# Kernel tuning notes

Hardware: AMD Instinct MI355X
Metric: run time of the kernel (lower is better)

## Reference

```python
import jax, jax.numpy as jnp
import numpy as np
from jax import lax

GAP_PENALTY = 0.0
TEMPERATURE = 1.0
B, A, L, D, K = 64, 26, 384, 512, 18


def setup_inputs() -> dict:
    key = jax.random.key(0)
    k1, k2, k3, k4 = jax.random.split(key, 4)
    matrices = jax.random.normal(k1, (B, A, L), dtype=jnp.float32)
    # ragged lengths: (len_i, len_0) per pair, in [L//2, L]
    shapes = jax.random.randint(k2, (B, 2), L // 2, L + 1, dtype=jnp.int32)
    s = 1.0 / np.sqrt(A * K)  # torch Conv1d default init scale
    conv_w = jax.random.uniform(k3, (D, A, K), minval=-s, maxval=s, dtype=jnp.float32)
    conv_b = jax.random.uniform(k4, (D,), minval=-s, maxval=s, dtype=jnp.float32)
    return {"matrices": matrices, "shapes": shapes, "conv_w": conv_w, "conv_b": conv_b}


def _smoothmax3(a, b, c, t):
    # t * log(exp(a/t) + exp(b/t) + exp(c/t)), numerically stable
    m = jnp.maximum(jnp.maximum(a, b), c)
    return m + t * jnp.log(jnp.exp((a - m) / t) + jnp.exp((b - m) / t) + jnp.exp((c - m) / t))


def _nw_matrix(sim, t, g):
    # sim: (L, L). Returns smoothed NW value matrix V: (L+1, L+1).
    # V[i,j] = sim[i-1,j-1] + smoothmax(V[i-1,j-1], V[i-1,j]-g, V[i,j-1]-g)
    n = sim.shape[0]
    row0 = -g * jnp.arange(n + 1, dtype=sim.dtype)  # free/affine leading gaps on top row

    def row_step(prev_row, inp):
        s_row, i = inp  # s_row: (L,)
        v_left0 = -g * i  # V[i, 0]

        def col_step(left, xs):
            s, diag, up = xs
            v = s + _smoothmax3(diag, up - g, left - g, t)
            return v, v

        _, rest = lax.scan(col_step, v_left0, (s_row, prev_row[:-1], prev_row[1:]))
        new_row = jnp.concatenate([v_left0[None], rest])
        return new_row, new_row

    _, rows = lax.scan(row_step, row0, (sim, jnp.arange(1, n + 1, dtype=sim.dtype)))
    return jnp.concatenate([row0[None], rows], axis=0)


def needleman_wunsch(sim, shapes, gap_penalty, temperature):
    # sim: (B, L, L) similarity vs sequence 0; shapes: (B, 2) int lengths.
    # Soft alignment posterior = grad of smoothed terminal score wrt similarity.
    li = jnp.clip(shapes[:, 0], 0, sim.shape[1])
    lj = jnp.clip(shapes[:, 1], 0, sim.shape[2])

    def total_score(s):
        V = jax.vmap(lambda m: _nw_matrix(m, temperature, gap_penalty))(s)  # (B, L+1, L+1)
        b = jnp.arange(s.shape[0])
        return jnp.sum(V[b, li, lj])

    return jax.grad(total_score)(sim)  # (B, L, L), expected match matrix


def reference(matrices, shapes, conv_w, conv_b):
    # Conv1d padding='same' with even kernel: torch pads (k-1)//2 left, k//2 right
    k = conv_w.shape[-1]
    pad = ((k - 1) // 2, k // 2)
    emb = lax.conv_general_dilated(
        matrices, conv_w, window_strides=(1,), padding=[pad],
        dimension_numbers=("NCH", "OIH", "NCH"),
    ) + conv_b[None, :, None]  # (B, D, L)
    e = jnp.transpose(emb, (0, 2, 1))  # (B, L, D)
    sim = jnp.einsum("bld,md->blm", e, e[0])  # (B, L_i, L_0): similarity vs sequence 0
    align = needleman_wunsch(sim, shapes, GAP_PENALTY, TEMPERATURE)  # (B, L, L)
    m = jnp.transpose(matrices, (0, 2, 1))  # (B, L, A)
    # consensus in sequence-0 coordinates, then project back to each sequence
    consensus = jnp.mean(jnp.einsum("nia,nij->nja", m, align), axis=0)  # (L, A)
    return jnp.einsum("ja,nij->nia", consensus, align)  # (B, L, A)
```

## Files before the change

kernel.cpp:

```cpp
#include <hip/hip_runtime.h>
#include <hip/hip_bf16.h>
#include <math.h>

#define B_  64
#define A_  26
#define L_  384
#define D_  512
#define K_  18
#define LP1 385
#define VS  384

typedef __attribute__((ext_vector_type(8))) short bf16x8;
typedef __attribute__((ext_vector_type(4))) float f32x4;
typedef unsigned short ushort_t;
typedef unsigned int uint_t;

__device__ __forceinline__ ushort_t f2bf(float v) {
    uint_t u = __float_as_uint(v);
    uint_t r = (u + 0x7FFFu + ((u >> 16) & 1u)) >> 16;
    return (ushort_t)r;
}

__device__ __forceinline__ float dpp_up1(float x) {
    return __int_as_float(__builtin_amdgcn_update_dpp(
        0, __float_as_int(x), 0x138, 0xF, 0xF, true));
}
__device__ __forceinline__ float dpp_down1(float x) {
    return __int_as_float(__builtin_amdgcn_update_dpp(
        0, __float_as_int(x), 0x130, 0xF, 0xF, true));
}

__global__ void transpose_w_kernel(const float* __restrict__ w, float* __restrict__ wt) {
    int o = blockIdx.x * blockDim.x + threadIdx.x;
    int total = A_ * K_ * D_;
    if (o >= total) return;
    int d = o % D_;
    int r = o / D_;
    wt[o] = w[(size_t)d * (A_ * K_) + r];
}

__global__ __launch_bounds__(512) void conv_kernel(const float* __restrict__ x,
                                                   const float* __restrict__ wt,
                                                   const float* __restrict__ bias,
                                                   ushort_t* __restrict__ ehi,
                                                   ushort_t* __restrict__ elo) {
    const int TL = 32;
    const int XW = TL + K_ - 1;
    int l0 = blockIdx.x * TL;
    int b  = blockIdx.y;
    int d  = threadIdx.x;
    __shared__ float xs[A_][XW];
    for (int idx = threadIdx.x; idx < A_ * XW; idx += 512) {
        int a = idx / XW, p = idx % XW;
        int g = l0 - (K_ - 1) / 2 + p;
        xs[a][p] = (g >= 0 && g < L_) ? x[((size_t)b * A_ + a) * L_ + g] : 0.0f;
    }
    __syncthreads();
    float acc[TL];
#pragma unroll
    for (int l = 0; l < TL; ++l) acc[l] = 0.0f;
#pragma unroll 1
    for (int a = 0; a < A_; ++a) {
        float xr[XW];
#pragma unroll
        for (int p = 0; p < XW; ++p) xr[p] = xs[a][p];
        const float* wrow = wt + (size_t)(a * K_) * D_ + d;
#pragma unroll
        for (int k = 0; k < K_; ++k) {
            float w = wrow[(size_t)k * D_];
#pragma unroll
            for (int l = 0; l < TL; ++l)
                acc[l] = fmaf(xr[k + l], w, acc[l]);
        }
    }
    float bv = bias[d];
#pragma unroll
    for (int l = 0; l < TL; ++l) {
        float v = acc[l] + bv;
        ushort_t h = f2bf(v);
        float hf = __uint_as_float(((uint_t)h) << 16);
        ushort_t lo = f2bf(v - hf);
        size_t idx = ((size_t)b * L_ + (l0 + l)) * D_ + d;
        ehi[idx] = h;
        elo[idx] = lo;
    }
}

__global__ __launch_bounds__(256) void sim_kernel(const ushort_t* __restrict__ ehi,
                                                  const ushort_t* __restrict__ elo,
                                                  float* __restrict__ sim) {
    int b = blockIdx.z;
    int w = threadIdx.x >> 6;
    int lane = threadIdx.x & 63;
    int l0 = blockIdx.y * 64 + 32 * (w >> 1);
    int m0 = blockIdx.x * 64 + 32 * (w & 1);
    int r = lane & 15, g = lane >> 4;
    size_t rowA = ((size_t)b * L_ + l0 + r) * D_ + g * 8;
    size_t rowB = ((size_t)m0 + r) * D_ + g * 8;
    const ushort_t* pah = ehi + rowA;
    const ushort_t* pal = elo + rowA;
    const ushort_t* pbh = ehi + rowB;
    const ushort_t* pbl = elo + rowB;
    f32x4 acc00 = {0.f, 0.f, 0.f, 0.f}, acc01 = acc00, acc10 = acc00, acc11 = acc00;
#pragma unroll 2
    for (int ks = 0; ks < 16; ++ks) {
        int off = ks * 32;
        bf16x8 Ah0 = *(const bf16x8*)(pah + off);
        bf16x8 Ah1 = *(const bf16x8*)(pah + 16 * D_ + off);
        bf16x8 Al0 = *(const bf16x8*)(pal + off);
        bf16x8 Al1 = *(const bf16x8*)(pal + 16 * D_ + off);
        bf16x8 Bh0 = *(const bf16x8*)(pbh + off);
        bf16x8 Bh1 = *(const bf16x8*)(pbh + 16 * D_ + off);
        bf16x8 Bl0 = *(const bf16x8*)(pbl + off);
        bf16x8 Bl1 = *(const bf16x8*)(pbl + 16 * D_ + off);
        acc00 = __builtin_amdgcn_mfma_f32_16x16x32_bf16(Ah0, Bh0, acc00, 0, 0, 0);
        acc00 = __builtin_amdgcn_mfma_f32_16x16x32_bf16(Ah0, Bl0, acc00, 0, 0, 0);
        acc00 = __builtin_amdgcn_mfma_f32_16x16x32_bf16(Al0, Bh0, acc00, 0, 0, 0);
        acc01 = __builtin_amdgcn_mfma_f32_16x16x32_bf16(Ah0, Bh1, acc01, 0, 0, 0);
        acc01 = __builtin_amdgcn_mfma_f32_16x16x32_bf16(Ah0, Bl1, acc01, 0, 0, 0);
        acc01 = __builtin_amdgcn_mfma_f32_16x16x32_bf16(Al0, Bh1, acc01, 0, 0, 0);
        acc10 = __builtin_amdgcn_mfma_f32_16x16x32_bf16(Ah1, Bh0, acc10, 0, 0, 0);
        acc10 = __builtin_amdgcn_mfma_f32_16x16x32_bf16(Ah1, Bl0, acc10, 0, 0, 0);
        acc10 = __builtin_amdgcn_mfma_f32_16x16x32_bf16(Al1, Bh0, acc10, 0, 0, 0);
        acc11 = __builtin_amdgcn_mfma_f32_16x16x32_bf16(Ah1, Bh1, acc11, 0, 0, 0);
        acc11 = __builtin_amdgcn_mfma_f32_16x16x32_bf16(Ah1, Bl1, acc11, 0, 0, 0);
        acc11 = __builtin_amdgcn_mfma_f32_16x16x32_bf16(Al1, Bh1, acc11, 0, 0, 0);
    }
    float* sp = sim + ((size_t)b * L_ + l0) * L_ + m0;
#pragma unroll
    for (int v = 0; v < 4; ++v) {
        int row = g * 4 + v;
        sp[(size_t)row * L_ + r]             = acc00[v];
        sp[(size_t)row * L_ + 16 + r]        = acc01[v];
        sp[(size_t)(16 + row) * L_ + r]      = acc10[v];
        sp[(size_t)(16 + row) * L_ + 16 + r] = acc11[v];
    }
}

__global__ __launch_bounds__(64, 1) void nw_fwd_kernel(const float* __restrict__ sim, float* __restrict__ V) {
    int b = blockIdx.x;
    int l = threadIdx.x;
    const float* sb = sim + (size_t)b * L_ * L_;
    float* Vb = V + (size_t)b * L_ * L_;
    const float* srow[6];
    float* vrow[6];
#pragma unroll
    for (int r = 0; r < 6; ++r) {
        srow[r] = sb + (size_t)(6 * l + r) * L_;
        vrow[r] = Vb + (size_t)(6 * l + r) * VS;
    }
    float vleft[6] = {0.f, 0.f, 0.f, 0.f, 0.f, 0.f};
    float bcarry[4] = {0.f, 0.f, 0.f, 0.f};
    float bprev = 0.f;

    auto body = [&](float4* buf, int T) {
        float sc[6][4];
#pragma unroll
        for (int r = 0; r < 6; ++r) {
            float4 t = buf[r];
            sc[r][0] = t.x; sc[r][1] = t.y; sc[r][2] = t.z; sc[r][3] = t.w;
        }
        int cP = min(max(4 * (T + 3 - l), 0), 380);
#pragma unroll
        for (int r = 0; r < 6; ++r) buf[r] = *(const float4*)(srow[r] + cP);
        float d0 = dpp_up1(bprev);
        float uin[4];
#pragma unroll
        for (int q = 0; q < 4; ++q) uin[q] = dpp_up1(bcarry[q]);
        int c0 = 4 * (T - l);
        if (c0 >= 0 && c0 <= 380) {
            float vout[6][4];
#pragma unroll
            for (int q = 0; q < 4; ++q) {
                float dg = (q == 0) ? d0 : uin[q - 1];
                float up = uin[q];
#pragma unroll
                for (int r = 0; r < 6; ++r) {
                    float lf = vleft[r];
                    float mx = fmaxf(dg, fmaxf(up, lf));
                    float v = sc[r][q] + mx + __logf(__expf(dg - mx) + __expf(up - mx) + __expf(lf - mx));
                    dg = lf;
                    up = v;
                    vleft[r] = v;
                    vout[r][q] = v;
                }
            }
            bprev = bcarry[3];
#pragma unroll
            for (int q = 0; q < 4; ++q) bcarry[q] = vout[5][q];
#pragma unroll
            for (int r = 0; r < 6; ++r) {
                float4 t;
                t.x = vout[r][0]; t.y = vout[r][1]; t.z = vout[r][2]; t.w = vout[r][3];
                *(float4*)(vrow[r] + c0) = t;
            }
        }
    };

    float4 buf0[6], buf1[6], buf2[6];
    {
        int cA = min(max(4 * (0 - l), 0), 380);
        int cB = min(max(4 * (1 - l), 0), 380);
        int cC = min(max(4 * (2 - l), 0), 380);
#pragma unroll
        for (int r = 0; r < 6; ++r) {
            buf0[r] = *(const float4*)(srow[r] + cA);
            buf1[r] = *(const float4*)(srow[r] + cB);
            buf2[r] = *(const float4*)(srow[r] + cC);
        }
    }
#pragma unroll 1
    for (int Tb = 0; Tb < 159; Tb += 3) {
        body(buf0, Tb);
        body(buf1, Tb + 1);
        body(buf2, Tb + 2);
    }
}

__global__ __launch_bounds__(64, 1) void nw_bwd_kernel(const float* __restrict__ sim,
                                                       const float* __restrict__ V,
                                                       const int* __restrict__ shapes,
                                                       float* __restrict__ align_) {
    int b = blockIdx.x;
    int l = threadIdx.x;
    const float* sb = sim + (size_t)b * L_ * L_;
    const float* Vb = V + (size_t)b * L_ * L_;
    float* ab = align_ + (size_t)b * L_ * L_;
    int li = min(max(shapes[2 * b + 0], 0), L_);
    int lj = min(max(shapes[2 * b + 1], 0), L_);
    __shared__ float Eb[2][388];
    __shared__ float Ub[2][388];
    for (int k = l; k < 2 * 388; k += 64) { ((float*)Eb)[k] = 0.f; ((float*)Ub)[k] = 0.f; }
    bool L63 = (l == 63);
#pragma unroll 1
    for (int pass = 0; pass < 3; ++pass) {
        int r0 = 256 - 128 * pass;
        int i1 = r0 + 2 * l + 1, i2 = i1 + 1;
        const float* pV0 = Vb + (size_t)(r0 + 2 * l) * VS;
        const float* pV1 = Vb + (size_t)(r0 + 2 * l + 1) * VS;
        const float* pS0 = sb + (size_t)(r0 + 2 * l) * L_;
        const float* pS1 = sb + (size_t)(r0 + 2 * l + 1) * L_;
        float* pE0 = ab + (size_t)(i1 - 1) * L_;
        float* pE1 = ab + (size_t)(i2 - 1) * L_;
        const float* Ebr = Eb[pass & 1];
        float* Ebw = Eb[(pass & 1) ^ 1];
        const float* Ubr = Ub[pass & 1];
        float* Ubw = Ub[(pass & 1) ^ 1];
        float e0 = 0.f, e1 = 0.f, u0p = 0.f, u1p = 0.f;
        float ecarry[4] = {0.f, 0.f, 0.f, 0.f};
        float ucarry[4] = {0.f, 0.f, 0.f, 0.f};
        float eprev_s = 0.f, uprev_s = 0.f;
        float eb_carry = 0.f, ub_carry = 0.f;

        auto body = [&](float4& fV0, float4& fV1, float4& fS0, float4& fS1, int T) {
            float V0q[4], V1q[4], S0q[4], S1q[4];
            { float4 t = fV0; V0q[0]=t.x; V0q[1]=t.y; V0q[2]=t.z; V0q[3]=t.w; }
            { float4 t = fV1; V1q[0]=t.x; V1q[1]=t.y; V1q[2]=t.z; V1q[3]=t.w; }
            { float4 t = fS0; S0q[0]=t.x; S0q[1]=t.y; S0q[2]=t.z; S0q[3]=t.w; }
            { float4 t = fS1; S1q[0]=t.x; S1q[1]=t.y; S1q[2]=t.z; S1q[3]=t.w; }
            int cP = min(max(380 - 4 * (T + 3 - (63 - l)), 0), 380);
            fV0 = *(const float4*)(pV0 + cP);
            fV1 = *(const float4*)(pV1 + cP);
            fS0 = *(const float4*)(pS0 + cP);
            fS1 = *(const float4*)(pS1 + cP);
            int c0 = 380 - 4 * (T - (63 - l));
            float enbtd3 = dpp_down1(eprev_s);
            float unbtd3 = dpp_down1(uprev_s);
            float enbc[4], unbc[4];
#pragma unroll
            for (int q = 0; q < 4; ++q) {
                enbc[q] = dpp_down1(ecarry[q]);
                unbc[q] = dpp_down1(ucarry[q]);
            }
            eprev_s = e0; uprev_s = u0p;
            if (c0 >= 0 && c0 <= 380) {
                float ebq[4] = {0.f, 0.f, 0.f, 0.f};
                float ubq[4] = {0.f, 0.f, 0.f, 0.f};
                if (L63) {
                    float4 t = *(const float4*)&Ebr[c0];
                    ebq[0] = t.x; ebq[1] = t.y; ebq[2] = t.z; ebq[3] = t.w;
                    float4 u = *(const float4*)&Ubr[c0];
                    ubq[0] = u.x; ubq[1] = u.y; ubq[2] = u.z; ubq[3] = u.w;
                }
                float u0c[4], u1c[4];
#pragma unroll
                for (int q = 0; q < 4; ++q) {
                    u0c[q] = V0q[q] - S0q[q];
                    u1c[q] = V1q[q] - S1q[q];
                }
                float Eo0[4], Eo1[4];
#pragma unroll
                for (int qq = 0; qq < 4; ++qq) {
                    const int q = 3 - qq;
                    int j = c0 + 1 + q;
                    float enb   = L63 ? ebq[q] : enbc[q];
                    float unb   = L63 ? ubq[q] : unbc[q];
                    float enbtd = (q == 3) ? (L63 ? eb_carry : enbtd3)
                                           : (L63 ? ebq[q + 1] : enbc[q + 1]);
                    float unbtd = (q == 3) ? (L63 ? ub_carry : unbtd3)
                                           : (L63 ? ubq[q + 1] : unbc[q + 1]);
                    bool jlt = (j < L_), i2lt = (i2 < L_);
                    float wtd1 = (i2lt && jlt) ? __expf(V1q[q] - unbtd) : 0.f;
                    float wtu1 = i2lt ? __expf(V1q[q] - unb) : 0.f;
                    float wtl1 = jlt ? __expf(V1q[q] - u1p) : 0.f;
                    float wtd0 = jlt ? __expf(V0q[q] - u1p) : 0.f;
                    float wtu0 = __expf(V0q[q] - u1c[q]);
                    float wtl0 = jlt ? __expf(V0q[q] - u0p) : 0.f;
                    float ea1 = (i2 == li && j == lj) ? 1.f : 0.f;
                    ea1 += wtd1 * enbtd + wtu1 * enb + wtl1 * e1;
                    float ea0 = (i1 == li && j == lj) ? 1.f : 0.f;
                    ea0 += wtd0 * e1 + wtu0 * ea1 + wtl0 * e0;
                    e1 = ea1; e0 = ea0;
                    u1p = u1c[q]; u0p = u0c[q];
                    Eo1[q] = ea1; Eo0[q] = ea0;
                }
                eb_carry = ebq[0]; ub_carry = ubq[0];
#pragma unroll
                for (int q = 0; q < 4; ++q) { ecarry[q] = Eo0[q]; ucarry[q] = u0c[q]; }
                float4 t0, t1;
                t0.x = Eo0[0]; t0.y = Eo0[1]; t0.z = Eo0[2]; t0.w = Eo0[3];
                t1.x = Eo1[0]; t1.y = Eo1[1]; t1.z = Eo1[2]; t1.w = Eo1[3];
                *(float4*)(pE0 + c0) = t0;
                *(float4*)(pE1 + c0) = t1;
                if (l == 0) {
                    *(float4*)&Ebw[c0] = t0;
                    float4 tu;
                    tu.x = u0c[0]; tu.y = u0c[1]; tu.z = u0c[2]; tu.w = u0c[3];
                    *(float4*)&Ubw[c0] = tu;
                }
            }
        };

        float4 aV0, aV1, aS0, aS1, bV0x, bV1x, bS0x, bS1x, cV0, cV1, cS0, cS1;
        {
            int c0p = min(max(380 - 4 * (0 - (63 - l)), 0), 380);
            int c1p = min(max(380 - 4 * (1 - (63 - l)), 0), 380);
            int c2p = min(max(380 - 4 * (2 - (63 - l)), 0), 380);
            aV0 = *(const float4*)(pV0 + c0p); aV1 = *(const float4*)(pV1 + c0p);
            aS0 = *(const float4*)(pS0 + c0p); aS1 = *(const float4*)(pS1 + c0p);
            bV0x = *(const float4*)(pV0 + c1p); bV1x = *(const float4*)(pV1 + c1p);
            bS0x = *(const float4*)(pS0 + c1p); bS1x = *(const float4*)(pS1 + c1p);
            cV0 = *(const float4*)(pV0 + c2p); cV1 = *(const float4*)(pV1 + c2p);
            cS0 = *(const float4*)(pS0 + c2p); cS1 = *(const float4*)(pS1 + c2p);
        }
#pragma unroll 1
        for (int Tb = 0; Tb < 159; Tb += 3) {
            body(aV0, aV1, aS0, aS1, Tb);
            body(bV0x, bV1x, bS0x, bS1x, Tb + 1);
            body(cV0, cV1, cS0, cS1, Tb + 2);
        }
    }
}

__global__ __launch_bounds__(256) void consensus_kernel(const float* __restrict__ x,
                                                        const float* __restrict__ align_,
                                                        float* __restrict__ cons) {
    int n  = blockIdx.y;
    int j0 = blockIdx.x * 64;
    __shared__ float ms[A_][L_];
    for (int idx = threadIdx.x; idx < A_ * L_; idx += 256)
        ((float*)ms)[idx] = x[(size_t)n * A_ * L_ + idx];
    __syncthreads();
    int jl = threadIdx.x & 63;
    int g  = threadIdx.x >> 6;
    int a0 = g * 7;
    int na = (a0 + 7 <= A_) ? 7 : (A_ - a0);
    int j  = j0 + jl;
    float acc[7] = {0.f, 0.f, 0.f, 0.f, 0.f, 0.f, 0.f};
    const float* acol = align_ + (size_t)n * L_ * L_ + j;
    for (int i = 0; i < L_; ++i) {
        float al = acol[(size_t)i * L_];
#pragma unroll
        for (int t = 0; t < 7; ++t)
            if (t < na) acc[t] = fmaf(al, ms[a0 + t][i], acc[t]);
    }
    for (int t = 0; t < na; ++t)
        atomicAdd(&cons[(size_t)j * A_ + a0 + t], acc[t] * (1.0f / B_));
}

__global__ __launch_bounds__(256) void out_kernel(const float* __restrict__ align_,
                                                  const float* __restrict__ cons,
                                                  float* __restrict__ out) {
    int n  = blockIdx.y;
    int i0 = blockIdx.x * 32;
    __shared__ float cs[L_][A_];
    __shared__ float as_[32][L_ + 1];
    for (int idx = threadIdx.x; idx < L_ * A_; idx += 256)
        ((float*)cs)[idx] = cons[idx];
    for (int idx = threadIdx.x; idx < 32 * L_; idx += 256) {
        int r = idx / L_, c = idx % L_;
        as_[r][c] = align_[((size_t)n * L_ + i0 + r) * L_ + c];
    }
    __syncthreads();
    for (int o = threadIdx.x; o < 32 * A_; o += 256) {
        int il = o / A_, a = o % A_;
        float s = 0.f;
        for (int jj = 0; jj < L_; ++jj)
            s = fmaf(as_[il][jj], cs[jj][a], s);
        out[((size_t)n * L_ + i0 + il) * A_ + a] = s;
    }
}

extern "C" void kernel_launch(void* const* d_in, const int* in_sizes, int n_in,
                              void* d_out, int out_size, void* d_ws, size_t ws_size,
                              hipStream_t stream) {
    const float* matrices = (const float*)d_in[0];
    const int*   shapes   = (const int*)d_in[1];
    const float* conv_w   = (const float*)d_in[2];
    const float* conv_b   = (const float*)d_in[3];
    float* out = (float*)d_out;

    char* p = (char*)d_ws;
    ushort_t* ehi = (ushort_t*)p;  p += (size_t)B_ * L_ * D_ * 2;
    ushort_t* elo = (ushort_t*)p;  p += (size_t)B_ * L_ * D_ * 2;
    float* sim    = (float*)p;     p += (size_t)B_ * L_ * L_ * 4;
    float* V      = (float*)p;     p += (size_t)B_ * L_ * L_ * 4;
    float* align_ = (float*)p;     p += (size_t)B_ * L_ * L_ * 4;
    float* wt     = (float*)p;     p += (size_t)A_ * K_ * D_ * 4;
    float* cons   = (float*)p;

    transpose_w_kernel<<<(A_ * K_ * D_ + 255) / 256, 256, 0, stream>>>(conv_w, wt);
    conv_kernel<<<dim3(L_ / 32, B_), 512, 0, stream>>>(matrices, wt, conv_b, ehi, elo);
    sim_kernel<<<dim3(L_ / 64, L_ / 64, B_), 256, 0, stream>>>(ehi, elo, sim);
    nw_fwd_kernel<<<B_, 64, 0, stream>>>(sim, V);
    nw_bwd_kernel<<<B_, 64, 0, stream>>>(sim, V, shapes, align_);
    hipMemsetAsync(cons, 0, (size_t)L_ * A_ * sizeof(float), stream);
    consensus_kernel<<<dim3(L_ / 64, B_), 256, 0, stream>>>(matrices, align_, cons);
    out_kernel<<<dim3(L_ / 32, B_), 256, 0, stream>>>(align_, cons, out);
}
```

Measured before the change: 1.046 ms.

## Store sim, V and alignment in wavefront-tiled layouts for coalesced NW access

Replaces the row-major sim, V and alignment buffers with custom tiled layouts (off_F for forward, off_B for backward). Each column-tile step of the NW wavefront then has all 64 lanes reading and writing contiguous float4 chunks instead of rows strided by L. The sim producer and the consensus and output consumers are rewritten to scatter into and gather from the new layouts. The cost is scattered stores in sim_kernel and more complex index math in the consumers.

```diff
diff --git a/kernel.cpp b/kernel.cpp
--- a/kernel.cpp
+++ b/kernel.cpp
@@ -7,13 +7,19 @@
 #define L_  384
 #define D_  512
 #define K_  18
-#define LP1 385
-#define VS  384
+#define LL  147456
 
 typedef __attribute__((ext_vector_type(8))) short bf16x8;
 typedef __attribute__((ext_vector_type(4))) float f32x4;
 typedef unsigned short ushort_t;
 typedef unsigned int uint_t;
+
+__device__ __forceinline__ int off_F(int z, int ct) {
+    return ((ct * 6 + z % 6) * 64 + z / 6) * 4;
+}
+__device__ __forceinline__ int off_B(int z, int ct) {
+    return ct * 1536 + ((z >> 7) << 9) + ((z & 1) << 8) + (((z & 127) >> 1) << 2);
+}
 
 __device__ __forceinline__ ushort_t f2bf(float v) {
     uint_t u = __float_as_uint(v);
@@ -88,7 +94,7 @@
 
 __global__ __launch_bounds__(256) void sim_kernel(const ushort_t* __restrict__ ehi,
                                                   const ushort_t* __restrict__ elo,
-                                                  float* __restrict__ sim) {
+                                                  float* __restrict__ simF) {
     int b = blockIdx.z;
     int w = threadIdx.x >> 6;
     int lane = threadIdx.x & 63;
@@ -126,29 +132,23 @@
         acc11 = __builtin_amdgcn_mfma_f32_16x16x32_bf16(Ah1, Bl1, acc11, 0, 0, 0);
         acc11 = __builtin_amdgcn_mfma_f32_16x16x32_bf16(Al1, Bh1, acc11, 0, 0, 0);
     }
-    float* sp = sim + ((size_t)b * L_ + l0) * L_ + m0;
+    float* sp = simF + (size_t)b * LL;
 #pragma unroll
     for (int v = 0; v < 4; ++v) {
-        int row = g * 4 + v;
-        sp[(size_t)row * L_ + r]             = acc00[v];
-        sp[(size_t)row * L_ + 16 + r]        = acc01[v];
-        sp[(size_t)(16 + row) * L_ + r]      = acc10[v];
-        sp[(size_t)(16 + row) * L_ + 16 + r] = acc11[v];
-    }
-}
-
-__global__ __launch_bounds__(64, 1) void nw_fwd_kernel(const float* __restrict__ sim, float* __restrict__ V) {
+        int ar0 = l0 + g * 4 + v, ar1 = ar0 + 16;
+        int ac0 = m0 + r,         ac1 = ac0 + 16;
+        sp[off_F(ar0, ac0 >> 2) + (ac0 & 3)] = acc00[v];
+        sp[off_F(ar0, ac1 >> 2) + (ac1 & 3)] = acc01[v];
+        sp[off_F(ar1, ac0 >> 2) + (ac0 & 3)] = acc10[v];
+        sp[off_F(ar1, ac1 >> 2) + (ac1 & 3)] = acc11[v];
+    }
+}
+
+__global__ __launch_bounds__(64, 1) void nw_fwd_kernel(const float* __restrict__ simF, float* __restrict__ VF) {
     int b = blockIdx.x;
     int l = threadIdx.x;
-    const float* sb = sim + (size_t)b * L_ * L_;
-    float* Vb = V + (size_t)b * L_ * L_;
-    const float* srow[6];
-    float* vrow[6];
-#pragma unroll
-    for (int r = 0; r < 6; ++r) {
-        srow[r] = sb + (size_t)(6 * l + r) * L_;
-        vrow[r] = Vb + (size_t)(6 * l + r) * VS;
-    }
+    const float* pS = simF + (size_t)b * LL + l * 4;
+    float*       pV = VF   + (size_t)b * LL + l * 4;
     float vleft[6] = {0.f, 0.f, 0.f, 0.f, 0.f, 0.f};
     float bcarry[4] = {0.f, 0.f, 0.f, 0.f};
     float bprev = 0.f;
@@ -160,15 +160,16 @@
             float4 t = buf[r];
             sc[r][0] = t.x; sc[r][1] = t.y; sc[r][2] = t.z; sc[r][3] = t.w;
         }
-        int cP = min(max(4 * (T + 3 - l), 0), 380);
-#pragma unroll
-        for (int r = 0; r < 6; ++r) buf[r] = *(const float4*)(srow[r] + cP);
+        int ctP = min(max(T + 3 - l, 0), 95);
+#pragma unroll
+        for (int r = 0; r < 6; ++r) buf[r] = *(const float4*)(pS + (ctP * 6 + r) * 256);
         float d0 = dpp_up1(bprev);
         float uin[4];
 #pragma unroll
         for (int q = 0; q < 4; ++q) uin[q] = dpp_up1(bcarry[q]);
         int c0 = 4 * (T - l);
         if (c0 >= 0 && c0 <= 380) {
+            int ct0 = c0 >> 2;
             float vout[6][4];
 #pragma unroll
             for (int q = 0; q < 4; ++q) {
@@ -192,21 +193,21 @@
             for (int r = 0; r < 6; ++r) {
                 float4 t;
                 t.x = vout[r][0]; t.y = vout[r][1]; t.z = vout[r][2]; t.w = vout[r][3];
-                *(float4*)(vrow[r] + c0) = t;
+                *(float4*)(pV + (ct0 * 6 + r) * 256) = t;
             }
         }
     };
 
     float4 buf0[6], buf1[6], buf2[6];
     {
-        int cA = min(max(4 * (0 - l), 0), 380);
-        int cB = min(max(4 * (1 - l), 0), 380);
-        int cC = min(max(4 * (2 - l), 0), 380);
+        int cA = min(max(0 - l, 0), 95);
+        int cB = min(max(1 - l, 0), 95);
+        int cC = min(max(2 - l, 0), 95);
 #pragma unroll
         for (int r = 0; r < 6; ++r) {
-            buf0[r] = *(const float4*)(srow[r] + cA);
-            buf1[r] = *(const float4*)(srow[r] + cB);
-            buf2[r] = *(const float4*)(srow[r] + cC);
+            buf0[r] = *(const float4*)(pS + (cA * 6 + r) * 256);
+            buf1[r] = *(const float4*)(pS + (cB * 6 + r) * 256);
+            buf2[r] = *(const float4*)(pS + (cC * 6 + r) * 256);
         }
     }
 #pragma unroll 1
@@ -217,15 +218,15 @@
     }
 }
 
-__global__ __launch_bounds__(64, 1) void nw_bwd_kernel(const float* __restrict__ sim,
-                                                       const float* __restrict__ V,
+__global__ __launch_bounds__(64, 1) void nw_bwd_kernel(const float* __restrict__ simF,
+                                                       const float* __restrict__ VF,
                                                        const int* __restrict__ shapes,
-                                                       float* __restrict__ align_) {
+                                                       float* __restrict__ alignB) {
     int b = blockIdx.x;
     int l = threadIdx.x;
-    const float* sb = sim + (size_t)b * L_ * L_;
-    const float* Vb = V + (size_t)b * L_ * L_;
-    float* ab = align_ + (size_t)b * L_ * L_;
+    const float* sB = simF + (size_t)b * LL;
+    const float* vB = VF   + (size_t)b * LL;
+    float* aB = alignB + (size_t)b * LL;
     int li = min(max(shapes[2 * b + 0], 0), L_);
     int lj = min(max(shapes[2 * b + 1], 0), L_);
     __shared__ float Eb[2][388];
@@ -236,12 +237,10 @@
     for (int pass = 0; pass < 3; ++pass) {
         int r0 = 256 - 128 * pass;
         int i1 = r0 + 2 * l + 1, i2 = i1 + 1;
-        const float* pV0 = Vb + (size_t)(r0 + 2 * l) * VS;
-        const float* pV1 = Vb + (size_t)(r0 + 2 * l + 1) * VS;
-        const float* pS0 = sb + (size_t)(r0 + 2 * l) * L_;
-        const float* pS1 = sb + (size_t)(r0 + 2 * l + 1) * L_;
-        float* pE0 = ab + (size_t)(i1 - 1) * L_;
-        float* pE1 = ab + (size_t)(i2 - 1) * L_;
+        int z0 = r0 + 2 * l;
+        int bo0 = off_F(z0, 0);
+        int bo1 = off_F(z0 + 1, 0);
+        float* pB0 = aB + ((2 - pass) << 9) + l * 4;
         const float* Ebr = Eb[pass & 1];
         float* Ebw = Eb[(pass & 1) ^ 1];
         const float* Ubr = Ub[pass & 1];
@@ -258,11 +257,11 @@
             { float4 t = fV1; V1q[0]=t.x; V1q[1]=t.y; V1q[2]=t.z; V1q[3]=t.w; }
             { float4 t = fS0; S0q[0]=t.x; S0q[1]=t.y; S0q[2]=t.z; S0q[3]=t.w; }
             { float4 t = fS1; S1q[0]=t.x; S1q[1]=t.y; S1q[2]=t.z; S1q[3]=t.w; }
-            int cP = min(max(380 - 4 * (T + 3 - (63 - l)), 0), 380);
-            fV0 = *(const float4*)(pV0 + cP);
-            fV1 = *(const float4*)(pV1 + cP);
-            fS0 = *(const float4*)(pS0 + cP);
-            fS1 = *(const float4*)(pS1 + cP);
+            int ctP = min(max(95 - (T + 3 - (63 - l)), 0), 95);
+            fV0 = *(const float4*)(vB + ctP * 1536 + bo0);
+            fV1 = *(const float4*)(vB + ctP * 1536 + bo1);
+            fS0 = *(const float4*)(sB + ctP * 1536 + bo0);
+            fS1 = *(const float4*)(sB + ctP * 1536 + bo1);
             int c0 = 380 - 4 * (T - (63 - l));
             float enbtd3 = dpp_down1(eprev_s);
             float unbtd3 = dpp_down1(uprev_s);
@@ -274,6 +273,7 @@
             }
             eprev_s = e0; uprev_s = u0p;
             if (c0 >= 0 && c0 <= 380) {
+                int ct0 = c0 >> 2;
                 float ebq[4] = {0.f, 0.f, 0.f, 0.f};
                 float ubq[4] = {0.f, 0.f, 0.f, 0.f};
                 if (L63) {
@@ -320,8 +320,8 @@
                 float4 t0, t1;
                 t0.x = Eo0[0]; t0.y = Eo0[1]; t0.z = Eo0[2]; t0.w = Eo0[3];
                 t1.x = Eo1[0]; t1.y = Eo1[1]; t1.z = Eo1[2]; t1.w = Eo1[3];
-                *(float4*)(pE0 + c0) = t0;
-                *(float4*)(pE1 + c0) = t1;
+                *(float4*)(pB0 + ct0 * 1536)       = t0;
+                *(float4*)(pB0 + 256 + ct0 * 1536) = t1;
                 if (l == 0) {
                     *(float4*)&Ebw[c0] = t0;
                     float4 tu;
@@ -333,15 +333,15 @@
 
         float4 aV0, aV1, aS0, aS1, bV0x, bV1x, bS0x, bS1x, cV0, cV1, cS0, cS1;
         {
-            int c0p = min(max(380 - 4 * (0 - (63 - l)), 0), 380);
-            int c1p = min(max(380 - 4 * (1 - (63 - l)), 0), 380);
-            int c2p = min(max(380 - 4 * (2 - (63 - l)), 0), 380);
-            aV0 = *(const float4*)(pV0 + c0p); aV1 = *(const float4*)(pV1 + c0p);
-            aS0 = *(const float4*)(pS0 + c0p); aS1 = *(const float4*)(pS1 + c0p);
-            bV0x = *(const float4*)(pV0 + c1p); bV1x = *(const float4*)(pV1 + c1p);
-            bS0x = *(const float4*)(pS0 + c1p); bS1x = *(const float4*)(pS1 + c1p);
-            cV0 = *(const float4*)(pV0 + c2p); cV1 = *(const float4*)(pV1 + c2p);
-            cS0 = *(const float4*)(pS0 + c2p); cS1 = *(const float4*)(pS1 + c2p);
+            int c0p = min(max(95 - (0 - (63 - l)), 0), 95);
+            int c1p = min(max(95 - (1 - (63 - l)), 0), 95);
+            int c2p = min(max(95 - (2 - (63 - l)), 0), 95);
+            aV0 = *(const float4*)(vB + c0p * 1536 + bo0); aV1 = *(const float4*)(vB + c0p * 1536 + bo1);
+            aS0 = *(const float4*)(sB + c0p * 1536 + bo0); aS1 = *(const float4*)(sB + c0p * 1536 + bo1);
+            bV0x = *(const float4*)(vB + c1p * 1536 + bo0); bV1x = *(const float4*)(vB + c1p * 1536 + bo1);
+            bS0x = *(const float4*)(sB + c1p * 1536 + bo0); bS1x = *(const float4*)(sB + c1p * 1536 + bo1);
+            cV0 = *(const float4*)(vB + c2p * 1536 + bo0); cV1 = *(const float4*)(vB + c2p * 1536 + bo1);
+            cS0 = *(const float4*)(sB + c2p * 1536 + bo0); cS1 = *(const float4*)(sB + c2p * 1536 + bo1);
         }
 #pragma unroll 1
         for (int Tb = 0; Tb < 159; Tb += 3) {
@@ -353,7 +353,7 @@
 }
 
 __global__ __launch_bounds__(256) void consensus_kernel(const float* __restrict__ x,
-                                                        const float* __restrict__ align_,
+                                                        const float* __restrict__ alignB,
                                                         float* __restrict__ cons) {
     int n  = blockIdx.y;
     int j0 = blockIdx.x * 64;
@@ -367,9 +367,9 @@
     int na = (a0 + 7 <= A_) ? 7 : (A_ - a0);
     int j  = j0 + jl;
     float acc[7] = {0.f, 0.f, 0.f, 0.f, 0.f, 0.f, 0.f};
-    const float* acol = align_ + (size_t)n * L_ * L_ + j;
+    const float* aB = alignB + (size_t)n * LL + ((j >> 2) * 1536 + (j & 3));
     for (int i = 0; i < L_; ++i) {
-        float al = acol[(size_t)i * L_];
+        float al = aB[((i >> 7) << 9) + ((i & 1) << 8) + (((i & 127) >> 1) << 2)];
 #pragma unroll
         for (int t = 0; t < 7; ++t)
             if (t < na) acc[t] = fmaf(al, ms[a0 + t][i], acc[t]);
@@ -378,7 +378,7 @@
         atomicAdd(&cons[(size_t)j * A_ + a0 + t], acc[t] * (1.0f / B_));
 }
 
-__global__ __launch_bounds__(256) void out_kernel(const float* __restrict__ align_,
+__global__ __launch_bounds__(256) void out_kernel(const float* __restrict__ alignB,
                                                   const float* __restrict__ cons,
                                                   float* __restrict__ out) {
     int n  = blockIdx.y;
@@ -387,9 +387,11 @@
     __shared__ float as_[32][L_ + 1];
     for (int idx = threadIdx.x; idx < L_ * A_; idx += 256)
         ((float*)cs)[idx] = cons[idx];
+    const float* aB = alignB + (size_t)n * LL;
     for (int idx = threadIdx.x; idx < 32 * L_; idx += 256) {
         int r = idx / L_, c = idx % L_;
-        as_[r][c] = align_[((size_t)n * L_ + i0 + r) * L_ + c];
+        int z = i0 + r;
+        as_[r][c] = aB[(c >> 2) * 1536 + ((z >> 7) << 9) + ((z & 1) << 8) + (((z & 127) >> 1) << 2) + (c & 3)];
     }
     __syncthreads();
     for (int o = threadIdx.x; o < 32 * A_; o += 256) {
@@ -413,18 +415,18 @@
     char* p = (char*)d_ws;
     ushort_t* ehi = (ushort_t*)p;  p += (size_t)B_ * L_ * D_ * 2;
     ushort_t* elo = (ushort_t*)p;  p += (size_t)B_ * L_ * D_ * 2;
-    float* sim    = (float*)p;     p += (size_t)B_ * L_ * L_ * 4;
-    float* V      = (float*)p;     p += (size_t)B_ * L_ * L_ * 4;
-    float* align_ = (float*)p;     p += (size_t)B_ * L_ * L_ * 4;
+    float* simF   = (float*)p;     p += (size_t)B_ * LL * 4;
+    float* VF     = (float*)p;     p += (size_t)B_ * LL * 4;
+    float* alignB = (float*)p;     p += (size_t)B_ * LL * 4;
     float* wt     = (float*)p;     p += (size_t)A_ * K_ * D_ * 4;
     float* cons   = (float*)p;
 
     transpose_w_kernel<<<(A_ * K_ * D_ + 255) / 256, 256, 0, stream>>>(conv_w, wt);
     conv_kernel<<<dim3(L_ / 32, B_), 512, 0, stream>>>(matrices, wt, conv_b, ehi, elo);
-    sim_kernel<<<dim3(L_ / 64, L_ / 64, B_), 256, 0, stream>>>(ehi, elo, sim);
-    nw_fwd_kernel<<<B_, 64, 0, stream>>>(sim, V);
-    nw_bwd_kernel<<<B_, 64, 0, stream>>>(sim, V, shapes, align_);
+    sim_kernel<<<dim3(L_ / 64, L_ / 64, B_), 256, 0, stream>>>(ehi, elo, simF);
+    nw_fwd_kernel<<<B_, 64, 0, stream>>>(simF, VF);
+    nw_bwd_kernel<<<B_, 64, 0, stream>>>(simF, VF, shapes, alignB);
     hipMemsetAsync(cons, 0, (size_t)L_ * A_ * sizeof(float), stream);
-    consensus_kernel<<<dim3(L_ / 64, B_), 256, 0, stream>>>(matrices, align_, cons);
-    out_kernel<<<dim3(L_ / 32, B_), 256, 0, stream>>>(align_, cons, out);
-}
+    consensus_kernel<<<dim3(L_ / 64, B_), 256, 0, stream>>>(matrices, alignB, cons);
+    out_kernel<<<dim3(L_ / 32, B_), 256, 0, stream>>>(alignB, cons, out);
+}
```

New measurement: 1.011 ms. 3.3% less time.
